# Performance work log

Measured on AMD Instinct MI355X. Metric: run time of the kernel, lower is better.

The kernel has to match this reference:

```python
import jax, jax.numpy as jnp
import numpy as np

N_P = 100000; N_F = 100000; N_PORT = 50000
F_IN = 64; H = 128; E = 200000; G = 128; OUT = 2


def setup_inputs() -> dict:
    key = jax.random.key(0)
    it = iter(jax.random.split(key, 64))
    def nrm(sh, s=1.0):
        return jax.random.normal(next(it), sh, jnp.float32) * s
    def ei(ns, nd):
        src = jax.random.randint(next(it), (E,), 0, ns)
        dst = jax.random.randint(next(it), (E,), 0, nd)
        return jnp.stack([src, dst]).astype(jnp.int32)
    def batch(n):
        return jnp.sort(jax.random.randint(next(it), (n,), 0, G)).astype(jnp.int32)
    return {
        'x_process': nrm((N_P, F_IN)), 'x_file': nrm((N_F, F_IN)), 'x_port': nrm((N_PORT, F_IN)),
        'W0': nrm((F_IN, H), 0.1), 'a0s': nrm((H,), 0.1), 'a0d': nrm((H,), 0.1), 'b0': jnp.zeros((H,), jnp.float32),
        'W1': nrm((H, H), 0.1), 'a1s': nrm((H,), 0.1), 'a1d': nrm((H,), 0.1), 'b1': jnp.zeros((H,), jnp.float32),
        'W2': nrm((H, H), 0.1), 'a2s': nrm((H,), 0.1), 'a2d': nrm((H,), 0.1), 'b2': jnp.zeros((H,), jnp.float32),
        'lin1_w': nrm((H, H), 0.1), 'lin1_b': jnp.zeros((H,), jnp.float32),
        'lin2_w': nrm((H, OUT), 0.1), 'lin2_b': jnp.zeros((OUT,), jnp.float32),
        'ei_access': ei(N_P, N_F), 'ei_rev_access': ei(N_F, N_P),
        'ei_same_as': ei(N_P, N_F), 'ei_rev_same_as': ei(N_F, N_P),
        'ei_bind': ei(N_P, N_PORT), 'ei_rev_bind': ei(N_PORT, N_P),
        'ei_session': ei(N_PORT, N_PORT), 'ei_rev_session': ei(N_PORT, N_PORT),
        'ei_create': ei(N_P, N_P), 'ei_rev_create': ei(N_P, N_P),
        'batch_process': batch(N_P), 'batch_file': batch(N_F), 'batch_port': batch(N_PORT),
    }


def _rel(h_src, s_src, d_dst, ei, b, n_dst):
    # single GATConv relation: gather, segment-softmax over dst, scatter-sum
    es, ed = ei[0], ei[1]
    alpha = jax.nn.leaky_relu(s_src[es] + d_dst[ed], 0.2)  # [E]
    m = jax.ops.segment_max(alpha, ed, num_segments=n_dst)
    m = jnp.where(jnp.isfinite(m), m, 0.0)
    ex = jnp.exp(alpha - m[ed])
    den = jax.ops.segment_sum(ex, ed, num_segments=n_dst)
    w = ex / jnp.maximum(den[ed], 1e-16)
    out = jax.ops.segment_sum(w[:, None] * h_src[es], ed, num_segments=n_dst)
    return out + b


def _forward(x_process, x_file, x_port,
             W0, a0s, a0d, b0, W1, a1s, a1d, b1, W2, a2s, a2d, b2,
             lin1_w, lin1_b, lin2_w, lin2_b,
             ei_access, ei_rev_access, ei_same_as, ei_rev_same_as,
             ei_bind, ei_rev_bind, ei_session, ei_rev_session,
             ei_create, ei_rev_create,
             batch_process, batch_file, batch_port):
    xp, xf, xpo = x_process, x_file, x_port
    for W, asr, adr, b in ((W0, a0s, a0d, b0), (W1, a1s, a1d, b1), (W2, a2s, a2d, b2)):
        # shared GATConv weights across all 10 relations -> transform each node type once
        hp, hf, hpo = xp @ W, xf @ W, xpo @ W
        sp, sf, spo = hp @ asr, hf @ asr, hpo @ asr
        dp, df, dpo = hp @ adr, hf @ adr, hpo @ adr
        # HeteroConv(aggr='mean'): average relation outputs per dst node type
        p_new = (_rel(hf, sf, dp, ei_rev_access, b, N_P)
                 + _rel(hf, sf, dp, ei_rev_same_as, b, N_P)
                 + _rel(hpo, spo, dp, ei_rev_bind, b, N_P)
                 + _rel(hp, sp, dp, ei_create, b, N_P)
                 + _rel(hp, sp, dp, ei_rev_create, b, N_P)) / 5.0
        f_new = (_rel(hp, sp, df, ei_access, b, N_F)
                 + _rel(hp, sp, df, ei_same_as, b, N_F)) / 2.0
        po_new = (_rel(hp, sp, dpo, ei_bind, b, N_PORT)
                  + _rel(hpo, spo, dpo, ei_session, b, N_PORT)
                  + _rel(hpo, spo, dpo, ei_rev_session, b, N_PORT)) / 3.0
        xp = jax.nn.leaky_relu(p_new, 0.01)
        xf = jax.nn.leaky_relu(f_new, 0.01)
        xpo = jax.nn.leaky_relu(po_new, 0.01)
    # pool_type == 1: global_add_pool over all node types concatenated
    x = jnp.concatenate([xp, xf, xpo], axis=0)
    bb = jnp.concatenate([batch_process, batch_file, batch_port], axis=0)
    pooled = jax.ops.segment_sum(x, bb, num_segments=G)  # [G, H]
    h = pooled @ lin1_w + lin1_b  # dropout is identity at eval
    return h @ lin2_w + lin2_b  # [G, OUT]


def reference(x_process, x_file, x_port,
              W0, a0s, a0d, b0, W1, a1s, a1d, b1, W2, a2s, a2d, b2,
              lin1_w, lin1_b, lin2_w, lin2_b,
              ei_access, ei_rev_access, ei_same_as, ei_rev_same_as,
              ei_bind, ei_rev_bind, ei_session, ei_rev_session,
              ei_create, ei_rev_create,
              batch_process, batch_file, batch_port):
    return _forward(x_process, x_file, x_port,
                    W0, a0s, a0d, b0, W1, a1s, a1d, b1, W2, a2s, a2d, b2,
                    lin1_w, lin1_b, lin2_w, lin2_b,
                    ei_access, ei_rev_access, ei_same_as, ei_rev_same_as,
                    ei_bind, ei_rev_bind, ei_session, ei_rev_session,
                    ei_create, ei_rev_create,
                    batch_process, batch_file, batch_port)
```

## Files before the change

kernel.cpp:

```cpp
#include <hip/hip_runtime.h>
#include <cstdint>
#include <cstddef>

#define E_EDGES 200000
#define NP 100000
#define NF 100000
#define NPORT 50000
#define NTOT 250000
#define TOTDEG 850000
#define GPOOL 128

typedef __attribute__((ext_vector_type(8))) short bf16x8;
typedef __attribute__((ext_vector_type(4))) float f32x4;

__device__ __forceinline__ float bf2f(unsigned short u) {
    return __uint_as_float(((unsigned int)u) << 16);
}
__device__ __forceinline__ unsigned short f2bf(float f) {
    unsigned int x = __float_as_uint(f);
    return (unsigned short)((x + 0x7fffu + ((x >> 16) & 1u)) >> 16);
}

struct EiPtrs {
    const int* p[10];
};

__device__ __forceinline__ int seg_of(int r, int dst) {
    if (r < 5) return dst * 5 + r;
    if (r < 7) return 500000 + dst * 2 + (r - 5);
    return 700000 + dst * 3 + (r - 7);
}
__device__ __forceinline__ int srcbase_of(int r) {
    return (r <= 1) ? 100000 : (r == 2 || r >= 8) ? 200000 : 0;
}

__global__ __launch_bounds__(256) void k_count_all(EiPtrs eis, int* __restrict__ deg) {
    int r = blockIdx.y;
    int e = blockIdx.x * 256 + threadIdx.x;
    if (e >= E_EDGES) return;
    atomicAdd(&deg[seg_of(r, eis.p[r][E_EDGES + e])], 1);
}

__global__ __launch_bounds__(256) void k_scan_partial(const int* __restrict__ deg,
                                                      int* __restrict__ bsum) {
    int t = threadIdx.x, b = blockIdx.x;
    int base = b * 1024 + t * 4;
    int sv = 0;
#pragma unroll
    for (int i = 0; i < 4; i++) {
        int idx = base + i;
        if (idx < TOTDEG) sv += deg[idx];
    }
#pragma unroll
    for (int msk = 1; msk < 64; msk <<= 1) sv += __shfl_xor(sv, msk);
    __shared__ int ws[4];
    if ((t & 63) == 0) ws[t >> 6] = sv;
    __syncthreads();
    if (t == 0) bsum[b] = ws[0] + ws[1] + ws[2] + ws[3];
}

__global__ __launch_bounds__(1024) void k_scan_bsums(int* __restrict__ bsum, int nb) {
    __shared__ int lds[1024];
    int t = threadIdx.x;
    int v = (t < nb) ? bsum[t] : 0;
    lds[t] = v;
    __syncthreads();
    for (int dd = 1; dd < 1024; dd <<= 1) {
        int u = (t >= dd) ? lds[t - dd] : 0;
        __syncthreads();
        lds[t] += u;
        __syncthreads();
    }
    if (t < nb) bsum[t] = lds[t] - v;
}

__global__ __launch_bounds__(256) void k_scan_final(const int* __restrict__ deg,
                                                    const int* __restrict__ bsum,
                                                    int* __restrict__ offs) {
    int t = threadIdx.x, b = blockIdx.x;
    int base = b * 1024 + t * 4;
    int v[4];
    int tot = 0;
#pragma unroll
    for (int i = 0; i < 4; i++) {
        int idx = base + i;
        v[i] = (idx < TOTDEG) ? deg[idx] : 0;
        tot += v[i];
    }
    int lane = t & 63, w = t >> 6;
    int x = tot;
#pragma unroll
    for (int dd = 1; dd < 64; dd <<= 1) {
        int u = __shfl_up(x, dd);
        if (lane >= dd) x += u;
    }
    __shared__ int wt[4];
    if (lane == 63) wt[w] = x;
    __syncthreads();
    int wbase = 0;
#pragma unroll
    for (int j = 0; j < 4; j++)
        if (j < w) wbase += wt[j];
    int run = bsum[b] + wbase + (x - tot);
#pragma unroll
    for (int i = 0; i < 4; i++) {
        int idx = base + i;
        if (idx <= TOTDEG) offs[idx] = run;
        run += v[i];
    }
}

__global__ __launch_bounds__(256) void k_fill_all(EiPtrs eis, const int* __restrict__ offs,
                                                  int* __restrict__ cursor,
                                                  int* __restrict__ list) {
    int r = blockIdx.y;
    int e = blockIdx.x * 256 + threadIdx.x;
    if (e >= E_EDGES) return;
    const int* ei = eis.p[r];
    int seg = seg_of(r, ei[E_EDGES + e]);
    int pos = atomicAdd(&cursor[seg], 1);
    list[offs[seg] + pos] = ei[e] + srcbase_of(r);
}

__global__ __launch_bounds__(256) void k_wt(const float* __restrict__ W,
                                            unsigned short* __restrict__ WT, int K) {
    int idx = blockIdx.x * 256 + threadIdx.x;
    if (idx >= 128 * K) return;
    int col = idx / K, k = idx - col * K;
    WT[idx] = f2bf(W[k * 128 + col]);
}

template <int K, bool BF16IN>
__global__ __launch_bounds__(256) void gemm_mfma(const void* __restrict__ xv,
                                                 const unsigned short* __restrict__ WT,
                                                 const float* __restrict__ avs,
                                                 const float* __restrict__ avd,
                                                 unsigned short* __restrict__ h,
                                                 float* __restrict__ s,
                                                 float* __restrict__ d, int N) {
    constexpr int NQ = K / 32;
    __shared__ float csmem[64][130];
    char* sw = (char*)&csmem[0][0];
    int tid = threadIdx.x;
    int w = tid >> 6, l = tid & 63;
    int row0 = blockIdx.x * 64;

    constexpr int WT_BYTES = 128 * K * 2;
#pragma unroll
    for (int i = tid * 16; i < WT_BYTES; i += 256 * 16) {
        uint4 v = *(const uint4*)((const char*)WT + i);
        int row = i / (2 * K);
        int addr = i ^ ((row & 7) << 4);
        *(uint4*)(sw + addr) = v;
    }

    int arow = row0 + w * 16 + (l & 15);
    bf16x8 afrag[NQ];
    if (arow < N) {
        if (BF16IN) {
            const unsigned short* x = (const unsigned short*)xv;
#pragma unroll
            for (int q = 0; q < NQ; ++q) {
                int kc = q * 32 + (l >> 4) * 8;
                afrag[q] = *(const bf16x8*)&x[(size_t)arow * K + kc];
            }
        } else {
            const float* x = (const float*)xv;
#pragma unroll
            for (int q = 0; q < NQ; ++q) {
                int kc = q * 32 + (l >> 4) * 8;
                float4 f0 = *(const float4*)&x[(size_t)arow * K + kc];
                float4 f1 = *(const float4*)&x[(size_t)arow * K + kc + 4];
                bf16x8 a;
                a[0] = (short)f2bf(f0.x);
                a[1] = (short)f2bf(f0.y);
                a[2] = (short)f2bf(f0.z);
                a[3] = (short)f2bf(f0.w);
                a[4] = (short)f2bf(f1.x);
                a[5] = (short)f2bf(f1.y);
                a[6] = (short)f2bf(f1.z);
                a[7] = (short)f2bf(f1.w);
                afrag[q] = a;
            }
        }
    } else {
#pragma unroll
        for (int q = 0; q < NQ; ++q) {
            bf16x8 z = {0, 0, 0, 0, 0, 0, 0, 0};
            afrag[q] = z;
        }
    }
    __syncthreads();

    f32x4 acc[8];
#pragma unroll
    for (int c = 0; c < 8; ++c) acc[c] = (f32x4){0.f, 0.f, 0.f, 0.f};

#pragma unroll
    for (int c = 0; c < 8; ++c) {
        int cabs = c * 16 + (l & 15);
        int base = cabs * (2 * K) + ((l >> 4) * 16);
        int swz = (cabs & 7) << 4;
#pragma unroll
        for (int q = 0; q < NQ; ++q) {
            int addr = (base + q * 64) ^ swz;
            bf16x8 b = *(const bf16x8*)(sw + addr);
            acc[c] = __builtin_amdgcn_mfma_f32_16x16x32_bf16(afrag[q], b, acc[c], 0, 0, 0);
        }
    }
    __syncthreads();

    int crow = w * 16 + (l >> 4) * 4;
    int ccol = l & 15;
#pragma unroll
    for (int c = 0; c < 8; ++c)
#pragma unroll
        for (int r = 0; r < 4; ++r) csmem[crow + r][c * 16 + ccol] = acc[c][r];
    __syncthreads();

    int row = tid >> 2, cg = tid & 3;
    int grow = row0 + row;
    if (grow < N) {
        float sv = 0.f, dv = 0.f;
        unsigned short tmp[32];
#pragma unroll
        for (int i = 0; i < 32; ++i) {
            float v = csmem[row][cg * 32 + i];
            sv = fmaf(v, avs[cg * 32 + i], sv);
            dv = fmaf(v, avd[cg * 32 + i], dv);
            tmp[i] = f2bf(v);
        }
        unsigned short* hp = &h[(size_t)grow * 128 + cg * 32];
        *(uint4*)&hp[0] = *(uint4*)&tmp[0];
        *(uint4*)&hp[8] = *(uint4*)&tmp[8];
        *(uint4*)&hp[16] = *(uint4*)&tmp[16];
        *(uint4*)&hp[24] = *(uint4*)&tmp[24];
        sv += __shfl_xor(sv, 1);
        sv += __shfl_xor(sv, 2);
        dv += __shfl_xor(dv, 1);
        dv += __shfl_xor(dv, 2);
        if (cg == 0) {
            s[grow] = sv;
            d[grow] = dv;
        }
    }
}

__global__ __launch_bounds__(256) void k_edgew(const int* __restrict__ offs,
                                               const int* __restrict__ list,
                                               const float* __restrict__ s_all,
                                               const float* __restrict__ d_all,
                                               unsigned short* __restrict__ wE) {
    int seg = blockIdx.x * 256 + threadIdx.x;
    if (seg >= TOTDEG) return;
    int o0 = offs[seg], o1 = offs[seg + 1];
    if (o1 == o0) return;
    int dst_g;
    if (seg < 500000)
        dst_g = seg / 5;
    else if (seg < 700000)
        dst_g = 100000 + (seg - 500000) / 2;
    else
        dst_g = 200000 + (seg - 700000) / 3;
    float dd = d_all[dst_g];
    float m = -1e30f, den = 0.f;
    for (int j = o0; j < o1; ++j) {
        float x = s_all[list[j]] + dd;
        x = (x >= 0.f) ? x : 0.2f * x;
        if (x > m) {
            den = den * __expf(m - x) + 1.f;
            m = x;
        } else {
            den += __expf(x - m);
        }
    }
    float invden = 1.f / fmaxf(den, 1e-16f);
    for (int j = o0; j < o1; ++j) {
        float x = s_all[list[j]] + dd;
        x = (x >= 0.f) ? x : 0.2f * x;
        wE[j] = f2bf(__expf(x - m) * invden);
    }
}

__global__ __launch_bounds__(256) void k_gather(const int* __restrict__ offs,
                                                const int* __restrict__ list,
                                                const unsigned short* __restrict__ wE,
                                                const float* __restrict__ bias,
                                                const unsigned short* __restrict__ H,
                                                unsigned short* __restrict__ X) {
    int grp = threadIdx.x >> 5, lane = threadIdx.x & 31;
    int dst = blockIdx.x * 8 + grp;
    if (dst >= NTOT) return;
    int seg0, nrel;
    float inv;
    if (dst < 100000) {
        seg0 = dst * 5;
        nrel = 5;
        inv = 0.2f;
    } else if (dst < 200000) {
        seg0 = 500000 + (dst - 100000) * 2;
        nrel = 2;
        inv = 0.5f;
    } else {
        seg0 = 700000 + (dst - 200000) * 3;
        nrel = 3;
        inv = 1.f / 3.f;
    }
    int o0 = offs[seg0], o1 = offs[seg0 + nrel];
    float a0 = 0.f, a1 = 0.f, a2 = 0.f, a3 = 0.f;
    float b0 = 0.f, b1 = 0.f, b2 = 0.f, b3 = 0.f;
    int j = o0;
    for (; j + 1 < o1; j += 2) {
        int s0 = list[j], s1 = list[j + 1];
        float w0 = bf2f(wE[j]), w1 = bf2f(wE[j + 1]);
        ushort4 h0 = *(const ushort4*)&H[(size_t)s0 * 128 + lane * 4];
        ushort4 h1 = *(const ushort4*)&H[(size_t)s1 * 128 + lane * 4];
        a0 = fmaf(w0, bf2f(h0.x), a0);
        a1 = fmaf(w0, bf2f(h0.y), a1);
        a2 = fmaf(w0, bf2f(h0.z), a2);
        a3 = fmaf(w0, bf2f(h0.w), a3);
        b0 = fmaf(w1, bf2f(h1.x), b0);
        b1 = fmaf(w1, bf2f(h1.y), b1);
        b2 = fmaf(w1, bf2f(h1.z), b2);
        b3 = fmaf(w1, bf2f(h1.w), b3);
    }
    if (j < o1) {
        int s0 = list[j];
        float w0 = bf2f(wE[j]);
        ushort4 h0 = *(const ushort4*)&H[(size_t)s0 * 128 + lane * 4];
        a0 = fmaf(w0, bf2f(h0.x), a0);
        a1 = fmaf(w0, bf2f(h0.y), a1);
        a2 = fmaf(w0, bf2f(h0.z), a2);
        a3 = fmaf(w0, bf2f(h0.w), a3);
    }
    a0 += b0;
    a1 += b1;
    a2 += b2;
    a3 += b3;
    float4 b4 = *(const float4*)&bias[lane * 4];
    float v0 = fmaf(a0, inv, b4.x);
    float v1 = fmaf(a1, inv, b4.y);
    float v2 = fmaf(a2, inv, b4.z);
    float v3 = fmaf(a3, inv, b4.w);
    v0 = (v0 >= 0.f) ? v0 : 0.01f * v0;
    v1 = (v1 >= 0.f) ? v1 : 0.01f * v1;
    v2 = (v2 >= 0.f) ? v2 : 0.01f * v2;
    v3 = (v3 >= 0.f) ? v3 : 0.01f * v3;
    ushort4 o;
    o.x = f2bf(v0);
    o.y = f2bf(v1);
    o.z = f2bf(v2);
    o.w = f2bf(v3);
    *(ushort4*)&X[(size_t)dst * 128 + lane * 4] = o;
}

__global__ __launch_bounds__(128) void pool_kernel(const unsigned short* __restrict__ x,
                                                   const int* __restrict__ batch,
                                                   float* __restrict__ pooled, int n) {
    int t = threadIdx.x;
    int start = blockIdx.x * 128;
    int end = min(start + 128, n);
    if (start >= n) return;
    float acc = 0.f;
    int g = batch[start];
    for (int i = start; i < end; ++i) {
        int gi = batch[i];
        if (gi != g) {
            atomicAdd(&pooled[(size_t)g * 128 + t], acc);
            acc = 0.f;
            g = gi;
        }
        acc += bf2f(x[(size_t)i * 128 + t]);
    }
    atomicAdd(&pooled[(size_t)g * 128 + t], acc);
}

__global__ __launch_bounds__(128) void k_mlp(const float* __restrict__ pooled,
                                             const float* __restrict__ w1,
                                             const float* __restrict__ b1,
                                             const float* __restrict__ w2,
                                             const float* __restrict__ b2,
                                             float* __restrict__ out) {
    __shared__ float p[128];
    __shared__ float r0[2], r1[2];
    int g = blockIdx.x, t = threadIdx.x;
    p[t] = pooled[g * 128 + t];
    __syncthreads();
    float acc = b1[t];
    for (int k = 0; k < 128; ++k) acc = fmaf(p[k], w1[k * 128 + t], acc);
    float v0 = acc * w2[t * 2 + 0];
    float v1 = acc * w2[t * 2 + 1];
#pragma unroll
    for (int msk = 1; msk < 64; msk <<= 1) {
        v0 += __shfl_xor(v0, msk);
        v1 += __shfl_xor(v1, msk);
    }
    if ((t & 63) == 0) {
        r0[t >> 6] = v0;
        r1[t >> 6] = v1;
    }
    __syncthreads();
    if (t == 0) {
        out[g * 2 + 0] = r0[0] + r0[1] + b2[0];
        out[g * 2 + 1] = r1[0] + r1[1] + b2[1];
    }
}

__global__ void k_ws_debug(float* out, int n, float val) {
    int i = blockIdx.x * 256 + threadIdx.x;
    if (i < n) out[i] = val;
}

extern "C" void kernel_launch(void* const* d_in, const int* in_sizes, int n_in,
                              void* d_out, int out_size, void* d_ws, size_t ws_size,
                              hipStream_t stream) {
    const float* x_p0 = (const float*)d_in[0];
    const float* x_f0 = (const float*)d_in[1];
    const float* x_po0 = (const float*)d_in[2];
    const float* Wl[3] = {(const float*)d_in[3], (const float*)d_in[7],
                          (const float*)d_in[11]};
    const float* asl[3] = {(const float*)d_in[4], (const float*)d_in[8],
                           (const float*)d_in[12]};
    const float* adl[3] = {(const float*)d_in[5], (const float*)d_in[9],
                           (const float*)d_in[13]};
    const float* bl[3] = {(const float*)d_in[6], (const float*)d_in[10],
                          (const float*)d_in[14]};
    const float* lin1_w = (const float*)d_in[15];
    const float* lin1_b = (const float*)d_in[16];
    const float* lin2_w = (const float*)d_in[17];
    const float* lin2_b = (const float*)d_in[18];
    EiPtrs eis;
    eis.p[0] = (const int*)d_in[20];
    eis.p[1] = (const int*)d_in[22];
    eis.p[2] = (const int*)d_in[24];
    eis.p[3] = (const int*)d_in[27];
    eis.p[4] = (const int*)d_in[28];
    eis.p[5] = (const int*)d_in[19];
    eis.p[6] = (const int*)d_in[21];
    eis.p[7] = (const int*)d_in[23];
    eis.p[8] = (const int*)d_in[25];
    eis.p[9] = (const int*)d_in[26];
    const int* batch_p = (const int*)d_in[29];
    const int* batch_f = (const int*)d_in[30];
    const int* batch_po = (const int*)d_in[31];
    float* out = (float*)d_out;

    char* w = (char*)d_ws;
    size_t off = 0;
    int* offs = (int*)(w + off);      off += (size_t)850004 * 4;
    int* cursor = (int*)(w + off);    off += (size_t)TOTDEG * 4;
    int* list = (int*)(w + off);      off += (size_t)10 * E_EDGES * 4;
    int* bsum = (int*)(w + off);      off += 4096;
    unsigned short* H = (unsigned short*)(w + off); off += (size_t)NTOT * 128 * 2;
    unsigned short* X = (unsigned short*)(w + off); off += (size_t)NTOT * 128 * 2;
    float* s_all = (float*)(w + off); off += (size_t)NTOT * 4;
    float* d_all = (float*)(w + off); off += (size_t)NTOT * 4;
    float* pooled = (float*)(w + off); off += (size_t)GPOOL * 128 * 4;
    unsigned short* WT0 = (unsigned short*)(w + off); off += (size_t)128 * 64 * 2;
    unsigned short* WT1 = (unsigned short*)(w + off); off += (size_t)128 * 128 * 2;
    unsigned short* WT2 = (unsigned short*)(w + off); off += (size_t)128 * 128 * 2;
    unsigned short* wE = (unsigned short*)(w + off); off += (size_t)10 * E_EDGES * 2;
    if (ws_size < off) {
        k_ws_debug<<<(out_size + 255) / 256, 256, 0, stream>>>(out, out_size,
                                                               (float)ws_size);
        return;
    }

    hipMemsetAsync(cursor, 0, (size_t)TOTDEG * 4, stream);
    hipMemsetAsync(pooled, 0, (size_t)GPOOL * 128 * 4, stream);

    k_wt<<<(128 * 64 + 255) / 256, 256, 0, stream>>>(Wl[0], WT0, 64);
    k_wt<<<(128 * 128 + 255) / 256, 256, 0, stream>>>(Wl[1], WT1, 128);
    k_wt<<<(128 * 128 + 255) / 256, 256, 0, stream>>>(Wl[2], WT2, 128);

    int eb = (E_EDGES + 255) / 256;
    k_count_all<<<dim3(eb, 10), 256, 0, stream>>>(eis, cursor);
    int nb = (TOTDEG + 1 + 1023) / 1024;
    k_scan_partial<<<nb, 256, 0, stream>>>(cursor, bsum);
    k_scan_bsums<<<1, 1024, 0, stream>>>(bsum, nb);
    k_scan_final<<<nb, 256, 0, stream>>>(cursor, bsum, offs);
    hipMemsetAsync(cursor, 0, (size_t)TOTDEG * 4, stream);
    k_fill_all<<<dim3(eb, 10), 256, 0, stream>>>(eis, offs, cursor, list);

    unsigned short* Hp = H;
    unsigned short* Hf = H + (size_t)NP * 128;
    unsigned short* Hpo = H + (size_t)(NP + NF) * 128;
    float* sp_ = s_all;
    float* sf_ = s_all + NP;
    float* spo_ = s_all + NP + NF;
    float* dp_ = d_all;
    float* df_ = d_all + NP;
    float* dpo_ = d_all + NP + NF;

    for (int L = 0; L < 3; ++L) {
        if (L == 0) {
            gemm_mfma<64, false><<<(NP + 63) / 64, 256, 0, stream>>>(
                x_p0, WT0, asl[0], adl[0], Hp, sp_, dp_, NP);
            gemm_mfma<64, false><<<(NF + 63) / 64, 256, 0, stream>>>(
                x_f0, WT0, asl[0], adl[0], Hf, sf_, df_, NF);
            gemm_mfma<64, false><<<(NPORT + 63) / 64, 256, 0, stream>>>(
                x_po0, WT0, asl[0], adl[0], Hpo, spo_, dpo_, NPORT);
        } else {
            const unsigned short* WTL = (L == 1) ? WT1 : WT2;
            gemm_mfma<128, true><<<(NTOT + 63) / 64, 256, 0, stream>>>(
                X, WTL, asl[L], adl[L], H, s_all, d_all, NTOT);
        }
        k_edgew<<<(TOTDEG + 255) / 256, 256, 0, stream>>>(offs, list, s_all, d_all, wE);
        k_gather<<<(NTOT + 7) / 8, 256, 0, stream>>>(offs, list, wE, bl[L], H, X);
    }

    unsigned short* Xp = X;
    unsigned short* Xf = X + (size_t)NP * 128;
    unsigned short* Xpo = X + (size_t)(NP + NF) * 128;
    pool_kernel<<<(NP + 127) / 128, 128, 0, stream>>>(Xp, batch_p, pooled, NP);
    pool_kernel<<<(NF + 127) / 128, 128, 0, stream>>>(Xf, batch_f, pooled, NF);
    pool_kernel<<<(NPORT + 127) / 128, 128, 0, stream>>>(Xpo, batch_po, pooled, NPORT);

    k_mlp<<<GPOOL, 128, 0, stream>>>(pooled, lin1_w, lin1_b, lin2_w, lin2_b, out);
}
```

Before: 921.5 us.

## Widen gather to wave-per-node, merge pooling kernels, seed fill cursor from offsets

The gather kernel now assigns one 64-lane wave per destination node, with each lane handling 2 columns, and unrolls the edge loop by 4 to keep more independent loads in flight. The three pooling launches are merged into a single kernel over all node types. The fill step now copies the scan offsets into the cursor instead of zeroing it, so the atomic returns the final list position and the extra offs read goes away. Narrower per-lane loads (4 bytes instead of 8) may lower memory efficiency per instruction.

```diff
diff --git a/kernel.cpp b/kernel.cpp
--- a/kernel.cpp
+++ b/kernel.cpp
@@ -16,6 +16,12 @@
 __device__ __forceinline__ float bf2f(unsigned short u) {
     return __uint_as_float(((unsigned int)u) << 16);
 }
+__device__ __forceinline__ float bf2f_lo(unsigned int r) {
+    return __uint_as_float(r << 16);
+}
+__device__ __forceinline__ float bf2f_hi(unsigned int r) {
+    return __uint_as_float(r & 0xffff0000u);
+}
 __device__ __forceinline__ unsigned short f2bf(float f) {
     unsigned int x = __float_as_uint(f);
     return (unsigned short)((x + 0x7fffu + ((x >> 16) & 1u)) >> 16);
@@ -110,7 +116,7 @@
     }
 }
 
-__global__ __launch_bounds__(256) void k_fill_all(EiPtrs eis, const int* __restrict__ offs,
+__global__ __launch_bounds__(256) void k_fill_all(EiPtrs eis,
                                                   int* __restrict__ cursor,
                                                   int* __restrict__ list) {
     int r = blockIdx.y;
@@ -119,7 +125,7 @@
     const int* ei = eis.p[r];
     int seg = seg_of(r, ei[E_EDGES + e]);
     int pos = atomicAdd(&cursor[seg], 1);
-    list[offs[seg] + pos] = ei[e] + srcbase_of(r);
+    list[pos] = ei[e] + srcbase_of(r);
 }
 
 __global__ __launch_bounds__(256) void k_wt(const float* __restrict__ W,
@@ -288,8 +294,8 @@
                                                 const float* __restrict__ bias,
                                                 const unsigned short* __restrict__ H,
                                                 unsigned short* __restrict__ X) {
-    int grp = threadIdx.x >> 5, lane = threadIdx.x & 31;
-    int dst = blockIdx.x * 8 + grp;
+    int wv = threadIdx.x >> 6, lane = threadIdx.x & 63;
+    int dst = blockIdx.x * 4 + wv;
     if (dst >= NTOT) return;
     int seg0, nrel;
     float inv;
@@ -307,70 +313,67 @@
         inv = 1.f / 3.f;
     }
     int o0 = offs[seg0], o1 = offs[seg0 + nrel];
-    float a0 = 0.f, a1 = 0.f, a2 = 0.f, a3 = 0.f;
-    float b0 = 0.f, b1 = 0.f, b2 = 0.f, b3 = 0.f;
+    int col2 = lane * 2;
+    float a0 = 0.f, a1 = 0.f, b0 = 0.f, b1 = 0.f;
+    float c0 = 0.f, c1 = 0.f, e0 = 0.f, e1 = 0.f;
     int j = o0;
-    for (; j + 1 < o1; j += 2) {
-        int s0 = list[j], s1 = list[j + 1];
+    for (; j + 3 < o1; j += 4) {
+        int s0 = list[j], s1 = list[j + 1], s2 = list[j + 2], s3 = list[j + 3];
         float w0 = bf2f(wE[j]), w1 = bf2f(wE[j + 1]);
-        ushort4 h0 = *(const ushort4*)&H[(size_t)s0 * 128 + lane * 4];
-        ushort4 h1 = *(const ushort4*)&H[(size_t)s1 * 128 + lane * 4];
-        a0 = fmaf(w0, bf2f(h0.x), a0);
-        a1 = fmaf(w0, bf2f(h0.y), a1);
-        a2 = fmaf(w0, bf2f(h0.z), a2);
-        a3 = fmaf(w0, bf2f(h0.w), a3);
-        b0 = fmaf(w1, bf2f(h1.x), b0);
-        b1 = fmaf(w1, bf2f(h1.y), b1);
-        b2 = fmaf(w1, bf2f(h1.z), b2);
-        b3 = fmaf(w1, bf2f(h1.w), b3);
-    }
-    if (j < o1) {
+        float w2 = bf2f(wE[j + 2]), w3 = bf2f(wE[j + 3]);
+        unsigned int r0 = *(const unsigned int*)&H[(size_t)s0 * 128 + col2];
+        unsigned int r1 = *(const unsigned int*)&H[(size_t)s1 * 128 + col2];
+        unsigned int r2 = *(const unsigned int*)&H[(size_t)s2 * 128 + col2];
+        unsigned int r3 = *(const unsigned int*)&H[(size_t)s3 * 128 + col2];
+        a0 = fmaf(w0, bf2f_lo(r0), a0);
+        a1 = fmaf(w0, bf2f_hi(r0), a1);
+        b0 = fmaf(w1, bf2f_lo(r1), b0);
+        b1 = fmaf(w1, bf2f_hi(r1), b1);
+        c0 = fmaf(w2, bf2f_lo(r2), c0);
+        c1 = fmaf(w2, bf2f_hi(r2), c1);
+        e0 = fmaf(w3, bf2f_lo(r3), e0);
+        e1 = fmaf(w3, bf2f_hi(r3), e1);
+    }
+    for (; j < o1; ++j) {
         int s0 = list[j];
         float w0 = bf2f(wE[j]);
-        ushort4 h0 = *(const ushort4*)&H[(size_t)s0 * 128 + lane * 4];
-        a0 = fmaf(w0, bf2f(h0.x), a0);
-        a1 = fmaf(w0, bf2f(h0.y), a1);
-        a2 = fmaf(w0, bf2f(h0.z), a2);
-        a3 = fmaf(w0, bf2f(h0.w), a3);
-    }
-    a0 += b0;
-    a1 += b1;
-    a2 += b2;
-    a3 += b3;
-    float4 b4 = *(const float4*)&bias[lane * 4];
-    float v0 = fmaf(a0, inv, b4.x);
-    float v1 = fmaf(a1, inv, b4.y);
-    float v2 = fmaf(a2, inv, b4.z);
-    float v3 = fmaf(a3, inv, b4.w);
+        unsigned int r0 = *(const unsigned int*)&H[(size_t)s0 * 128 + col2];
+        a0 = fmaf(w0, bf2f_lo(r0), a0);
+        a1 = fmaf(w0, bf2f_hi(r0), a1);
+    }
+    a0 += b0 + c0 + e0;
+    a1 += b1 + c1 + e1;
+    float2 bb = *(const float2*)&bias[col2];
+    float v0 = fmaf(a0, inv, bb.x);
+    float v1 = fmaf(a1, inv, bb.y);
     v0 = (v0 >= 0.f) ? v0 : 0.01f * v0;
     v1 = (v1 >= 0.f) ? v1 : 0.01f * v1;
-    v2 = (v2 >= 0.f) ? v2 : 0.01f * v2;
-    v3 = (v3 >= 0.f) ? v3 : 0.01f * v3;
-    ushort4 o;
-    o.x = f2bf(v0);
-    o.y = f2bf(v1);
-    o.z = f2bf(v2);
-    o.w = f2bf(v3);
-    *(ushort4*)&X[(size_t)dst * 128 + lane * 4] = o;
-}
-
-__global__ __launch_bounds__(128) void pool_kernel(const unsigned short* __restrict__ x,
-                                                   const int* __restrict__ batch,
-                                                   float* __restrict__ pooled, int n) {
+    unsigned int o = ((unsigned int)f2bf(v1) << 16) | f2bf(v0);
+    *(unsigned int*)&X[(size_t)dst * 128 + col2] = o;
+}
+
+__global__ __launch_bounds__(128) void pool_all(const unsigned short* __restrict__ X,
+                                                const int* __restrict__ bp,
+                                                const int* __restrict__ bf,
+                                                const int* __restrict__ bpo,
+                                                float* __restrict__ pooled) {
     int t = threadIdx.x;
     int start = blockIdx.x * 128;
-    int end = min(start + 128, n);
-    if (start >= n) return;
+    int end = min(start + 128, NTOT);
+    if (start >= end) return;
+    auto bat = [&](int i) {
+        return (i < NP) ? bp[i] : (i < NP + NF) ? bf[i - NP] : bpo[i - NP - NF];
+    };
     float acc = 0.f;
-    int g = batch[start];
+    int g = bat(start);
     for (int i = start; i < end; ++i) {
-        int gi = batch[i];
+        int gi = bat(i);
         if (gi != g) {
             atomicAdd(&pooled[(size_t)g * 128 + t], acc);
             acc = 0.f;
             g = gi;
         }
-        acc += bf2f(x[(size_t)i * 128 + t]);
+        acc += bf2f(X[(size_t)i * 128 + t]);
     }
     atomicAdd(&pooled[(size_t)g * 128 + t], acc);
 }
@@ -479,8 +482,8 @@
     k_scan_partial<<<nb, 256, 0, stream>>>(cursor, bsum);
     k_scan_bsums<<<1, 1024, 0, stream>>>(bsum, nb);
     k_scan_final<<<nb, 256, 0, stream>>>(cursor, bsum, offs);
-    hipMemsetAsync(cursor, 0, (size_t)TOTDEG * 4, stream);
-    k_fill_all<<<dim3(eb, 10), 256, 0, stream>>>(eis, offs, cursor, list);
+    hipMemcpyAsync(cursor, offs, (size_t)TOTDEG * 4, hipMemcpyDeviceToDevice, stream);
+    k_fill_all<<<dim3(eb, 10), 256, 0, stream>>>(eis, cursor, list);
 
     unsigned short* Hp = H;
     unsigned short* Hf = H + (size_t)NP * 128;
@@ -506,15 +509,11 @@
                 X, WTL, asl[L], adl[L], H, s_all, d_all, NTOT);
         }
         k_edgew<<<(TOTDEG + 255) / 256, 256, 0, stream>>>(offs, list, s_all, d_all, wE);
-        k_gather<<<(NTOT + 7) / 8, 256, 0, stream>>>(offs, list, wE, bl[L], H, X);
-    }
-
-    unsigned short* Xp = X;
-    unsigned short* Xf = X + (size_t)NP * 128;
-    unsigned short* Xpo = X + (size_t)(NP + NF) * 128;
-    pool_kernel<<<(NP + 127) / 128, 128, 0, stream>>>(Xp, batch_p, pooled, NP);
-    pool_kernel<<<(NF + 127) / 128, 128, 0, stream>>>(Xf, batch_f, pooled, NF);
-    pool_kernel<<<(NPORT + 127) / 128, 128, 0, stream>>>(Xpo, batch_po, pooled, NPORT);
+        k_gather<<<(NTOT + 3) / 4, 256, 0, stream>>>(offs, list, wE, bl[L], H, X);
+    }
+
+    pool_all<<<(NTOT + 127) / 128, 128, 0, stream>>>(X, batch_p, batch_f, batch_po,
+                                                     pooled);
 
     k_mlp<<<GPOOL, 128, 0, stream>>>(pooled, lin1_w, lin1_b, lin2_w, lin2_b, out);
 }
```

Result: slower. 987.3 us (+7.1%).
